# Kernel optimization log

Hardware: AMD Instinct MI355X
Metric: run time of the kernel (lower is better)

The kernel has to match this reference:

```python
import jax, jax.numpy as jnp
import numpy as np

EPS = 1e-12  # F.normalize clamp


def setup_inputs() -> dict:
    key = jax.random.key(0)
    features = jax.random.normal(key, (8192, 256), dtype=jnp.float32)
    return {"features": features}


def reference(features) -> jnp.ndarray:
    # F.normalize(features, dim=1)
    norm = jnp.maximum(jnp.linalg.norm(features, axis=1, keepdims=True), EPS)
    f = features / norm
    sim = f @ f.T  # [2B, 2B]
    n = sim.shape[0]
    b = n // 2
    idx = jnp.arange(n)
    # positive pair index: idx+B for first half, idx-B for second half
    pos_idx = jnp.where(idx < b, idx + b, idx - b)
    pos = sim[idx, pos_idx]  # sim with the positive example
    # CE with target 0 over logits row [pos, negatives (all j != i, j != pos)]:
    # denominator = exp(pos) + sum_{j != i, j != pos} exp(sim_ij) = sum_{j != i} exp(sim_ij)
    self_mask = idx[:, None] == idx[None, :]
    masked = jnp.where(self_mask, -jnp.inf, sim)
    lse = jax.nn.logsumexp(masked, axis=1)
    loss = jnp.mean(lse - pos)
    return loss
```

## Files before the change

### kernel.cpp

```cpp
#include <hip/hip_runtime.h>
#include <hip/hip_bf16.h>
#include <stdint.h>

#define N 8192
#define D 256
#define ROWB 128
#define COLG 16
#define COLS_PER_BLK (N / COLG)
#define CTILE 32
#define NT (COLS_PER_BLK / CTILE)
#define TILE_BYTES (CTILE * D)
#define NBUF 4
#define E_CONST 2.71828182845904523536f

typedef __attribute__((ext_vector_type(4))) int i32x4;
typedef __attribute__((ext_vector_type(8))) int i32x8;
typedef __attribute__((ext_vector_type(16))) float f32x16;

typedef const __attribute__((address_space(1))) void gvoid_t;
typedef __attribute__((address_space(3))) void lvoid_t;
__device__ inline void gload_lds16(const void* g, void* l) {
  __builtin_amdgcn_global_load_lds((gvoid_t*)g, (lvoid_t*)l, 16, 0, 0);
}

#if !__has_builtin(__builtin_amdgcn_cvt_pk_fp8_f32)
__device__ inline unsigned int f2e4m3(float x) {
  union { float f; unsigned u; } c; c.f = x;
  unsigned s = (c.u >> 31) << 7;
  float ax = fabsf(x);
  if (!(ax > 0.0f)) return s;
  if (ax >= 448.0f) return s | 0x7E;
  int e; float m = frexpf(ax, &e);
  int E = e - 1 + 7;
  if (E <= 0) {
    int qi = (int)rintf(ax * 512.0f);
    if (qi > 7) return s | 0x08;
    return s | (unsigned)qi;
  }
  int qi = (int)rintf(m * 16.0f);
  if (qi == 16) { qi = 8; E += 1; }
  if (E > 15) return s | 0x7E;
  return s | (unsigned)((E << 3) | (qi - 8));
}
#endif

__global__ __launch_bounds__(256) void norm_kernel(const float* __restrict__ feat,
                                                   unsigned char* __restrict__ f8,
                                                   float* __restrict__ pos,
                                                   float* __restrict__ out) {
  __shared__ float4 sh[4][64];
  int wave = threadIdx.x >> 6, lane = threadIdx.x & 63;
  int base = blockIdx.x << 1;
  int row = (wave < 2) ? (base + wave) : (4096 + base + (wave - 2));
  const float4 v = *(const float4*)(feat + (size_t)row * D + lane * 4);
  float ss = v.x * v.x + v.y * v.y + v.z * v.z + v.w * v.w;
  for (int m = 1; m < 64; m <<= 1) ss += __shfl_xor(ss, m, 64);
  float rn = 1.0f / fmaxf(sqrtf(ss), 1e-12f);
  float4 nv = make_float4(v.x * rn, v.y * rn, v.z * rn, v.w * rn);
#if __has_builtin(__builtin_amdgcn_cvt_pk_fp8_f32)
  int p = __builtin_amdgcn_cvt_pk_fp8_f32(nv.x, nv.y, 0, 0);
  p = __builtin_amdgcn_cvt_pk_fp8_f32(nv.z, nv.w, p, 1);
#else
  int p = (int)(f2e4m3(nv.x) | (f2e4m3(nv.y) << 8) |
                (f2e4m3(nv.z) << 16) | (f2e4m3(nv.w) << 24));
#endif
  *(int*)(f8 + (size_t)row * D + lane * 4) = p;
  sh[wave][lane] = nv;
  __syncthreads();
  if (wave < 2) {
    float4 q = sh[wave + 2][lane];
    float d = nv.x * q.x + nv.y * q.y + nv.z * q.z + nv.w * q.w;
    for (int m = 1; m < 64; m <<= 1) d += __shfl_xor(d, m, 64);
    if (lane == 0) {
      pos[base + wave] = d;
      pos[4096 + base + wave] = d;
    }
  }
  if (blockIdx.x == 0 && threadIdx.x == 0) out[0] = 0.0f;
}

__global__ __launch_bounds__(256, 3) void simlse_kernel(const unsigned char* __restrict__ f8,
                                                        float* __restrict__ slab) {
  __shared__ char lds[NBUF * TILE_BYTES];
  const char* fb = (const char*)f8;
  int tid = threadIdx.x;
  int wave = tid >> 6, lane = tid & 63;
  int c31 = lane & 31, h = lane >> 5;
  int rb = blockIdx.x >> 4;
  int cg = blockIdx.x & 15;
  int rowbase = rb * ROWB + wave * 32;

  i32x8 a[4];
  {
    const char* ar = fb + (size_t)(rowbase + c31) * D + h * 32;
#pragma unroll
    for (int m = 0; m < 4; ++m) {
      i32x4 lo = *(const i32x4*)(ar + m * 64);
      i32x4 hi = *(const i32x4*)(ar + m * 64 + 16);
      a[m] = __builtin_shufflevector(lo, hi, 0, 1, 2, 3, 4, 5, 6, 7);
    }
  }
#pragma unroll
  for (int m = 0; m < 4; ++m)
    asm volatile("" : "+v"(a[m]));

  float srow[16];
#pragma unroll
  for (int r = 0; r < 16; ++r) srow[r] = 0.0f;

  int colbase = cg * COLS_PER_BLK;
  int o0 = tid * 16, o1 = o0 + 4096;
  int r0 = o0 >> 8, r1 = o1 >> 8;
  int g0 = (o0 & 255) ^ ((r0 & 7) << 4);
  int g1 = (o1 & 255) ^ ((r1 & 7) << 4);
  int sw = (c31 & 7) << 4;

#define STAGE(tt)                                                              \
  {                                                                            \
    char* stg = lds + ((tt) & (NBUF - 1)) * TILE_BYTES;                        \
    size_t cb = (size_t)(colbase + (tt) * CTILE);                              \
    gload_lds16(fb + (cb + r0) * D + g0, stg + wave * 1024);                   \
    gload_lds16(fb + (cb + r1) * D + g1, stg + 4096 + wave * 1024);            \
  }

#define COMPUTE(tt)                                                            \
  {                                                                            \
    const char* bb = lds + ((tt) & (NBUF - 1)) * TILE_BYTES + c31 * 256;       \
    f32x16 acc = {0, 0, 0, 0, 0, 0, 0, 0, 0, 0, 0, 0, 0, 0, 0, 0};            \
    _Pragma("unroll")                                                          \
    for (int m = 0; m < 4; ++m) {                                              \
      int base = m * 64 + h * 32;                                              \
      i32x4 lo = *(const i32x4*)(bb + (base ^ sw));                            \
      i32x4 hi = *(const i32x4*)(bb + ((base + 16) ^ sw));                     \
      i32x8 bv = __builtin_shufflevector(lo, hi, 0, 1, 2, 3, 4, 5, 6, 7);      \
      acc = __builtin_amdgcn_mfma_scale_f32_32x32x64_f8f6f4(                   \
          a[m], bv, acc, 0, 0, 0, 127, 0, 127);                                \
    }                                                                          \
    _Pragma("unroll")                                                          \
    for (int r = 0; r < 16; ++r) srow[r] += __expf(acc[r]);                    \
  }

  STAGE(0);
  STAGE(1);

  const int NP = NT / 2;
  for (int u = 0; u < NP; ++u) {
    asm volatile("s_waitcnt vmcnt(0)" ::: "memory");
    __builtin_amdgcn_sched_barrier(0);
    __builtin_amdgcn_s_barrier();
    __builtin_amdgcn_sched_barrier(0);
    if (u + 1 < NP) {
      STAGE(2 * u + 2);
      STAGE(2 * u + 3);
    }
    COMPUTE(2 * u);
    COMPUTE(2 * u + 1);
  }
#undef STAGE
#undef COMPUTE

#pragma unroll
  for (int r = 0; r < 16; ++r) {
    srow[r] += __shfl_xor(srow[r], 1, 64);
    srow[r] += __shfl_xor(srow[r], 2, 64);
    srow[r] += __shfl_xor(srow[r], 4, 64);
    srow[r] += __shfl_xor(srow[r], 8, 64);
    srow[r] += __shfl_xor(srow[r], 16, 64);
  }
  if (c31 == 0) {
#pragma unroll
    for (int r = 0; r < 16; ++r) {
      int grow = rowbase + (r & 3) + 8 * (r >> 2) + 4 * h;
      slab[(size_t)cg * N + grow] = srow[r];
    }
  }
}

__global__ __launch_bounds__(256) void final_kernel(const float* __restrict__ slab,
                                                    const float* __restrict__ pos,
                                                    float* __restrict__ out) {
  int tid = threadIdx.x;
  int row = blockIdx.x * 256 + tid;
  float ssum = 0.0f;
#pragma unroll
  for (int c = 0; c < COLG; ++c) ssum += slab[(size_t)c * N + row];
  float v = __logf(ssum - E_CONST) - pos[row];
  for (int m = 1; m < 64; m <<= 1) v += __shfl_xor(v, m, 64);
  __shared__ float r4[4];
  if ((tid & 63) == 0) r4[tid >> 6] = v;
  __syncthreads();
  if (tid == 0)
    atomicAdd(out, (r4[0] + r4[1] + r4[2] + r4[3]) * (1.0f / (float)N));
}

extern "C" void kernel_launch(void* const* d_in, const int* in_sizes, int n_in,
                              void* d_out, int out_size, void* d_ws, size_t ws_size,
                              hipStream_t stream) {
  const float* feat = (const float*)d_in[0];
  unsigned char* f8 = (unsigned char*)d_ws;
  float* pos  = (float*)((char*)d_ws + (size_t)N * D);
  float* slab = (float*)((char*)d_ws + (size_t)N * D + (size_t)N * 4);
  float* out = (float*)d_out;

  norm_kernel<<<N / 4, 256, 0, stream>>>(feat, f8, pos, out);
  simlse_kernel<<<(N / ROWB) * COLG, 256, 0, stream>>>(f8, slab);
  final_kernel<<<N / 256, 256, 0, stream>>>(slab, pos, out);
}
```

Before: 33.72 us.

## Software-pipeline MFMA tiles with delayed exp accumulation in fully unrolled loop

Fully unrolls the tile loop and splits each tile's work into an MFMA phase and an exp-accumulate phase. The exp/add for the previous pair of tiles is interleaved with the MFMAs of the current pair, using double-buffered accumulators. The goal is to hide MFMA latency and keep the matrix and vector ALUs busy at the same time. It costs 32 extra accumulator VGPRs, which could hurt occupancy under the 3-wave launch bound, and it hardcodes the tile count at 16.

```diff
diff --git a/kernel.cpp b/kernel.cpp
--- a/kernel.cpp
+++ b/kernel.cpp
@@ -115,6 +115,8 @@
   int g1 = (o1 & 255) ^ ((r1 & 7) << 4);
   int sw = (c31 & 7) << 4;
 
+  f32x16 pA, pB, qA, qB;
+
 #define STAGE(tt)                                                              \
   {                                                                            \
     char* stg = lds + ((tt) & (NBUF - 1)) * TILE_BYTES;                        \
@@ -123,41 +125,57 @@
     gload_lds16(fb + (cb + r1) * D + g1, stg + 4096 + wave * 1024);            \
   }
 
-#define COMPUTE(tt)                                                            \
+#define MFMA_TILE(tt, ACC)                                                     \
   {                                                                            \
     const char* bb = lds + ((tt) & (NBUF - 1)) * TILE_BYTES + c31 * 256;       \
-    f32x16 acc = {0, 0, 0, 0, 0, 0, 0, 0, 0, 0, 0, 0, 0, 0, 0, 0};            \
+    ACC = (f32x16){0, 0, 0, 0, 0, 0, 0, 0, 0, 0, 0, 0, 0, 0, 0, 0};           \
     _Pragma("unroll")                                                          \
     for (int m = 0; m < 4; ++m) {                                              \
       int base = m * 64 + h * 32;                                              \
       i32x4 lo = *(const i32x4*)(bb + (base ^ sw));                            \
       i32x4 hi = *(const i32x4*)(bb + ((base + 16) ^ sw));                     \
       i32x8 bv = __builtin_shufflevector(lo, hi, 0, 1, 2, 3, 4, 5, 6, 7);      \
-      acc = __builtin_amdgcn_mfma_scale_f32_32x32x64_f8f6f4(                   \
-          a[m], bv, acc, 0, 0, 0, 127, 0, 127);                                \
+      ACC = __builtin_amdgcn_mfma_scale_f32_32x32x64_f8f6f4(                   \
+          a[m], bv, ACC, 0, 0, 0, 127, 0, 127);                                \
     }                                                                          \
+  }
+
+#define EXPADD(ACC)                                                            \
+  {                                                                            \
     _Pragma("unroll")                                                          \
-    for (int r = 0; r < 16; ++r) srow[r] += __expf(acc[r]);                    \
-  }
-
-  STAGE(0);
-  STAGE(1);
-
-  const int NP = NT / 2;
-  for (int u = 0; u < NP; ++u) {
-    asm volatile("s_waitcnt vmcnt(0)" ::: "memory");
-    __builtin_amdgcn_sched_barrier(0);
-    __builtin_amdgcn_s_barrier();
-    __builtin_amdgcn_sched_barrier(0);
-    if (u + 1 < NP) {
-      STAGE(2 * u + 2);
-      STAGE(2 * u + 3);
-    }
-    COMPUTE(2 * u);
-    COMPUTE(2 * u + 1);
-  }
+    for (int r = 0; r < 16; ++r) srow[r] += __expf(ACC[r]);                    \
+  }
+
+#define SYNC()                                                                 \
+  asm volatile("s_waitcnt vmcnt(0)" ::: "memory");                             \
+  __builtin_amdgcn_sched_barrier(0);                                           \
+  __builtin_amdgcn_s_barrier();                                                \
+  __builtin_amdgcn_sched_barrier(0);
+
+  STAGE(0); STAGE(1);
+
+  SYNC(); STAGE(2); STAGE(3);
+  MFMA_TILE(0, qA); MFMA_TILE(1, qB);
+  SYNC(); STAGE(4); STAGE(5);
+  MFMA_TILE(2, pA); EXPADD(qA); MFMA_TILE(3, pB); EXPADD(qB);
+  SYNC(); STAGE(6); STAGE(7);
+  MFMA_TILE(4, qA); EXPADD(pA); MFMA_TILE(5, qB); EXPADD(pB);
+  SYNC(); STAGE(8); STAGE(9);
+  MFMA_TILE(6, pA); EXPADD(qA); MFMA_TILE(7, pB); EXPADD(qB);
+  SYNC(); STAGE(10); STAGE(11);
+  MFMA_TILE(8, qA); EXPADD(pA); MFMA_TILE(9, qB); EXPADD(pB);
+  SYNC(); STAGE(12); STAGE(13);
+  MFMA_TILE(10, pA); EXPADD(qA); MFMA_TILE(11, pB); EXPADD(qB);
+  SYNC(); STAGE(14); STAGE(15);
+  MFMA_TILE(12, qA); EXPADD(pA); MFMA_TILE(13, qB); EXPADD(pB);
+  SYNC();
+  MFMA_TILE(14, pA); EXPADD(qA); MFMA_TILE(15, pB); EXPADD(qB);
+  EXPADD(pA); EXPADD(pB);
+
 #undef STAGE
-#undef COMPUTE
+#undef MFMA_TILE
+#undef EXPADD
+#undef SYNC
 
 #pragma unroll
   for (int r = 0; r < 16; ++r) {
```

Result: slower. 62.89 us (+86.5%).
